# Kernel tuning notes

Hardware: AMD Instinct MI355X
Metric: run time of the kernel (lower is better)

## Reference

```python
import jax, jax.numpy as jnp
import numpy as np

N, T, K, C, O = 2048, 20, 32, 32, 64  # agents, timesteps, neighbors, in_ch, out_ch


def setup_inputs() -> dict:
    key = jax.random.key(0)
    ks = jax.random.split(key, 8)
    s = 0.05
    x = jax.random.normal(ks[0], (N, T, C), dtype=jnp.float32)
    A = jax.random.randint(ks[1], (T, N, K), 0, N)  # neighbor indices into agent dim
    conv_w = jax.random.normal(ks[2], (O, C), jnp.float32) * s  # 1x1 conv == linear [O,C]
    conv_b = jax.random.normal(ks[3], (O,), jnp.float32) * s
    w_ih = jax.random.normal(ks[4], (4 * O, O), jnp.float32) * s  # LSTM gates i,f,g,o
    w_hh = jax.random.normal(ks[5], (4 * O, O), jnp.float32) * s
    b_ih = jax.random.normal(ks[6], (4 * O,), jnp.float32) * s
    b_hh = jax.random.normal(ks[7], (4 * O,), jnp.float32) * s
    return dict(x=x, A=A, conv_w=conv_w, conv_b=conv_b,
                w_ih=w_ih, w_hh=w_hh, b_ih=b_ih, b_hh=b_hh)


def reference(x, A, conv_w, conv_b, w_ih, w_hh, b_ih, b_hh):
    n = x.shape[0]
    xt = jnp.transpose(x, (1, 0, 2))  # [T, N, C]
    # align == 1: per-timestep neighbor gather and relative difference
    gathered = jax.vmap(lambda xs, idx: xs[idx])(xt, A)  # [T, N, K, C]
    diff = gathered - xt[:, :, None, :]  # [T, N, K, C]
    # 1x1 conv (pointwise linear over channels)
    y = jnp.einsum('tnkc,oc->tnko', diff, conv_w) + conv_b  # [T, N, K, O]
    # AdaptiveMaxPool2d((seq_len, 1)): max over the neighbor axis K
    feat = jnp.max(y, axis=2)  # [T, N, O] -- LSTM input (time-major)

    h0 = jnp.zeros((n, O), jnp.float32)
    c0 = jnp.zeros((n, O), jnp.float32)

    def step(carry, x_t):
        h, c = carry
        g = x_t @ w_ih.T + h @ w_hh.T + (b_ih + b_hh)  # [N, 4O]
        i_g, f_g, g_g, o_g = jnp.split(g, 4, axis=-1)
        c = jax.nn.sigmoid(f_g) * c + jax.nn.sigmoid(i_g) * jnp.tanh(g_g)
        h = jax.nn.sigmoid(o_g) * jnp.tanh(c)
        return (h, c), h

    (hN, cN), hs = jax.lax.scan(step, (h0, c0), feat)
    out = jnp.transpose(hs, (1, 0, 2))  # [N, T, O]
    # state_tuple permuted to batch-first as in the torch module
    return out, hN[:, None, :], cN[:, None, :]
```

## Files before the change

kernel.cpp:

```cpp
#include <hip/hip_runtime.h>
#include <hip/hip_bf16.h>
#include <math.h>

#define NA 2048
#define TT 20
#define KK 32
#define CC 32
#define OO 64
#define GG 256

typedef __attribute__((ext_vector_type(8))) short short8;
typedef __attribute__((ext_vector_type(4))) float float4v;

__device__ __forceinline__ float fast_rcp(float x) {
    return __builtin_amdgcn_rcpf(x);
}
__device__ __forceinline__ float sigm(float x) {
    return fast_rcp(1.f + __expf(-x));
}
__device__ __forceinline__ float tanh_fast(float x) {
    return 1.f - 2.f * fast_rcp(1.f + __expf(2.f * x));
}
__device__ __forceinline__ unsigned cvt_rne(float f) {
    unsigned u = __float_as_uint(f);
    return (u + 0x7FFFu + ((u >> 16) & 1u)) >> 16;
}
__device__ __forceinline__ unsigned pack2(float a, float b) {
    return cvt_rne(a) | (cvt_rne(b) << 16);
}
__device__ __forceinline__ float bf_lo(unsigned u) {
    return __uint_as_float(u << 16);
}
__device__ __forceinline__ float bf_hi(unsigned u) {
    return __uint_as_float(u & 0xffff0000u);
}

__global__ __launch_bounds__(256) void proj_kernel(
    const float* __restrict__ x, const float* __restrict__ conv_w,
    const float* __restrict__ conv_b, const float* __restrict__ w_ih,
    const float* __restrict__ w_hh, const float* __restrict__ b_ih,
    const float* __restrict__ b_hh,
    __hip_bfloat16* __restrict__ P, unsigned short* __restrict__ wihb,
    unsigned short* __restrict__ whhb, float* __restrict__ biasT)
{
    const int tid = threadIdx.x;
    if (blockIdx.x == 0) {
        for (int e = tid; e < 4 * OO * OO; e += 256) {
            wihb[e] = (unsigned short)cvt_rne(w_ih[e]);
            whhb[e] = (unsigned short)cvt_rne(w_hh[e]);
        }
        float bj = b_ih[tid] + b_hh[tid];
        #pragma unroll
        for (int o = 0; o < OO; o += 4) {
            float4 cb = *(const float4*)(conv_b + o);
            float4 wr = *(const float4*)(w_ih + (size_t)tid * OO + o);
            bj = fmaf(cb.x, wr.x, bj); bj = fmaf(cb.y, wr.y, bj);
            bj = fmaf(cb.z, wr.z, bj); bj = fmaf(cb.w, wr.w, bj);
        }
        biasT[tid] = bj;
        return;
    }
    const int lane = tid & 63;
    const int wv = tid >> 6;
    float w[CC];
    #pragma unroll
    for (int c = 0; c < CC; c += 4) {
        float4 v = *(const float4*)(conv_w + lane * CC + c);
        w[c] = v.x; w[c + 1] = v.y; w[c + 2] = v.z; w[c + 3] = v.w;
    }
    const int rbase = (blockIdx.x - 1) * 16 + wv * 4;
    #pragma unroll
    for (int i = 0; i < 4; ++i) {
        int r = rbase + i;
        const float* xr = x + (size_t)r * CC;
        float a0 = 0.f, a1 = 0.f;
        #pragma unroll
        for (int c = 0; c < CC; c += 8) {
            float4 v = *(const float4*)(xr + c);
            float4 u = *(const float4*)(xr + c + 4);
            a0 = fmaf(v.x, w[c], a0);     a0 = fmaf(v.y, w[c + 1], a0);
            a0 = fmaf(v.z, w[c + 2], a0); a0 = fmaf(v.w, w[c + 3], a0);
            a1 = fmaf(u.x, w[c + 4], a1); a1 = fmaf(u.y, w[c + 5], a1);
            a1 = fmaf(u.z, w[c + 6], a1); a1 = fmaf(u.w, w[c + 7], a1);
        }
        int n = r / TT;
        int t = r - n * TT;
        ((unsigned short*)P)[(((size_t)t << 11) + n) * OO + lane] =
            (unsigned short)cvt_rne(a0 + a1);
    }
}

__global__ __launch_bounds__(256, 4) void gather_kernel(
    const __hip_bfloat16* __restrict__ P, const int* __restrict__ A,
    unsigned* __restrict__ featw)
{
    __shared__ int A_sh[4][128];
    const int tid = threadIdx.x;
    const int lane = tid & 63;
    const int wv = tid >> 6;
    const int bs = (blockIdx.x & 7) * 320 + (blockIdx.x >> 3);
    const int r0 = bs << 4;
    const int t = r0 >> 11;
    const unsigned short* Pt = (const unsigned short*)P + ((size_t)t << 17);

    const int rw = r0 + wv * 4;
    ((int2*)A_sh[wv])[lane] = ((const int2*)(A + ((size_t)rw << 5)))[lane];

    const int i_row = lane >> 4;
    const int oc8 = lane & 15;
    const char* plane = (const char*)Pt + oc8 * 8;
    const int* myA = &A_sh[wv][i_row * 32];

    const int nself = (rw + i_row) & (NA - 1);
    const uint2 su = *(const uint2*)(plane + ((size_t)nself << 7));

    float m0 = -INFINITY, m1 = -INFINITY, m2 = -INFINITY, m3 = -INFINITY;
    #pragma unroll
    for (int bb = 0; bb < 2; ++bb) {
        int idx[16];
        #pragma unroll
        for (int g = 0; g < 16; ++g)
            idx[g] = myA[bb * 16 + g];
        uint2 uv[16];
        #pragma unroll
        for (int g = 0; g < 16; ++g)
            uv[g] = *(const uint2*)(plane + ((size_t)idx[g] << 7));
        #pragma unroll
        for (int g = 0; g < 16; ++g) {
            m0 = fmaxf(m0, bf_lo(uv[g].x)); m1 = fmaxf(m1, bf_hi(uv[g].x));
            m2 = fmaxf(m2, bf_lo(uv[g].y)); m3 = fmaxf(m3, bf_hi(uv[g].y));
        }
    }
    uint2 pk;
    pk.x = pack2(m0 - bf_lo(su.x), m1 - bf_hi(su.x));
    pk.y = pack2(m2 - bf_lo(su.y), m3 - bf_hi(su.y));
    *(uint2*)&featw[((size_t)(rw + i_row) << 5) + oc8 * 2] = pk;
}

__global__ __launch_bounds__(256) void lstm_kernel(
    const unsigned short* __restrict__ feat,
    const unsigned short* __restrict__ wihb,
    const unsigned short* __restrict__ whhb,
    const float* __restrict__ biasT, float* __restrict__ out)
{
    const int tid = threadIdx.x;
    const int lane = tid & 63;
    const int wv = tid >> 6;
    const int l15 = lane & 15;
    const int q = lane >> 4;
    const int a0 = blockIdx.x * 16;
    const int ch = wv * 16 + l15;

    short8 bfI[4][2], bfH[4][2];
    #pragma unroll
    for (int g = 0; g < 4; ++g) {
        int row = g * 64 + ch;
        #pragma unroll
        for (int ks = 0; ks < 2; ++ks) {
            bfI[g][ks] =
                *(const short8*)(wihb + ((size_t)row << 6) + ks * 32 + q * 8);
            bfH[g][ks] =
                *(const short8*)(whhb + ((size_t)row << 6) + ks * 32 + q * 8);
        }
    }
    float bias_g[4];
    #pragma unroll
    for (int g = 0; g < 4; ++g)
        bias_g[g] = biasT[g * 64 + ch];

    __shared__ __align__(16) unsigned short h_sh[2][16 * 72];

    for (int e = tid; e < 16 * 72 / 2; e += 256)
        ((unsigned*)h_sh[0])[e] = 0u;

    float cst[4] = {0.f, 0.f, 0.f, 0.f};

    short8 ff[2];
    #pragma unroll
    for (int ks = 0; ks < 2; ++ks)
        ff[ks] = *(const short8*)(
            feat + (((size_t)a0 + l15) << 6) + ks * 32 + q * 8);

    __syncthreads();

    for (int t = 0; t < TT; ++t) {
        short8 ah[2];
        #pragma unroll
        for (int ks = 0; ks < 2; ++ks)
            ah[ks] = *(const short8*)(
                &h_sh[t & 1][l15 * 72 + ks * 32 + q * 8]);

        float4v acc[4] = {{0.f, 0.f, 0.f, 0.f}, {0.f, 0.f, 0.f, 0.f},
                          {0.f, 0.f, 0.f, 0.f}, {0.f, 0.f, 0.f, 0.f}};
        #pragma unroll
        for (int ks = 0; ks < 2; ++ks) {
            #pragma unroll
            for (int g = 0; g < 4; ++g) {
                acc[g] = __builtin_amdgcn_mfma_f32_16x16x32_bf16(
                    ff[ks], bfI[g][ks], acc[g], 0, 0, 0);
                acc[g] = __builtin_amdgcn_mfma_f32_16x16x32_bf16(
                    ah[ks], bfH[g][ks], acc[g], 0, 0, 0);
            }
        }

        short8 ffn[2];
        int tn = (t + 1 < TT) ? t + 1 : t;
        #pragma unroll
        for (int ks = 0; ks < 2; ++ks)
            ffn[ks] = *(const short8*)(
                feat + ((((size_t)tn << 11) + a0 + l15) << 6) + ks * 32 + q * 8);

        #pragma unroll
        for (int rg = 0; rg < 4; ++rg) {
            float gi = acc[0][rg] + bias_g[0];
            float gf = acc[1][rg] + bias_g[1];
            float gz = acc[2][rg] + bias_g[2];
            float go = acc[3][rg] + bias_g[3];
            float ig = sigm(gi);
            float fg = sigm(gf);
            float zg = tanh_fast(gz);
            float og = sigm(go);
            cst[rg] = fmaf(fg, cst[rg], ig * zg);
            float hv = og * tanh_fast(cst[rg]);
            int agent = q * 4 + rg;
            h_sh[(t + 1) & 1][agent * 72 + ch] = (unsigned short)cvt_rne(hv);
            out[(((size_t)(a0 + agent) * TT + t) << 6) + ch] = hv;
            if (t == TT - 1) {
                size_t hb = (size_t)NA * TT * OO;
                out[hb + ((size_t)(a0 + agent) << 6) + ch] = hv;
                out[hb + ((size_t)NA << 6) + ((size_t)(a0 + agent) << 6) + ch] =
                    cst[rg];
            }
        }
        __syncthreads();
        ff[0] = ffn[0]; ff[1] = ffn[1];
    }
}

extern "C" void kernel_launch(void* const* d_in, const int* in_sizes, int n_in,
                              void* d_out, int out_size, void* d_ws, size_t ws_size,
                              hipStream_t stream) {
    const float* x      = (const float*)d_in[0];
    const int*   A      = (const int*)  d_in[1];
    const float* conv_w = (const float*)d_in[2];
    const float* conv_b = (const float*)d_in[3];
    const float* w_ih   = (const float*)d_in[4];
    const float* w_hh   = (const float*)d_in[5];
    const float* b_ih   = (const float*)d_in[6];
    const float* b_hh   = (const float*)d_in[7];
    float* out = (float*)d_out;

    char* ws = (char*)d_ws;
    __hip_bfloat16* P  = (__hip_bfloat16*)ws;
    size_t offF = (size_t)TT * NA * OO * 2;
    unsigned* featw = (unsigned*)(ws + offF);
    size_t offW = offF + (size_t)TT * NA * OO * 2;
    unsigned short* wihb = (unsigned short*)(ws + offW);
    unsigned short* whhb = wihb + 4 * OO * OO;
    float* biasT = (float*)(whhb + 4 * OO * OO);

    hipLaunchKernelGGL(proj_kernel, dim3(NA * TT / 16 + 1), dim3(256), 0, stream,
                       x, conv_w, conv_b, w_ih, w_hh, b_ih, b_hh,
                       P, wihb, whhb, biasT);
    hipLaunchKernelGGL(gather_kernel, dim3(NA * TT / 16), dim3(256), 0, stream,
                       P, A, featw);
    hipLaunchKernelGGL(lstm_kernel, dim3(NA / 16), dim3(256), 0, stream,
                       (const unsigned short*)featw, wihb, whhb, biasT, out);
}
```

Measured before the change: 130.2 us.

## Fuse gather and LSTM kernels with per-timestep flags for producer-consumer overlap

Merges the gather and LSTM kernels into one launch. The first NGRP blocks run the recurrent LSTM and spin on per-(timestep, agent-group) flags, and the remaining blocks perform the neighbor gather-max and publish a release flag when each tile is written. The LSTM's early timesteps can then overlap with gathers for later timesteps, and one kernel launch boundary disappears. The cost is spin-wait polling, atomic feature loads, and a reliance on the LSTM blocks and gather blocks being co-resident, which risks deadlock or stalls if the scheduler does not dispatch producers.

```diff
diff --git a/kernel.cpp b/kernel.cpp
--- a/kernel.cpp
+++ b/kernel.cpp
@@ -9,6 +9,10 @@
 #define OO 64
 #define GG 256
 
+#define NGRP (NA / 16)
+#define NGATH (NA * TT / 16)
+#define FLG_STRIDE 32
+
 typedef __attribute__((ext_vector_type(8))) short short8;
 typedef __attribute__((ext_vector_type(4))) float float4v;
 
@@ -33,6 +37,22 @@
 }
 __device__ __forceinline__ float bf_hi(unsigned u) {
     return __uint_as_float(u & 0xffff0000u);
+}
+
+__device__ __forceinline__ void wait_flag(const unsigned* f) {
+    while (__hip_atomic_load(f, __ATOMIC_RELAXED,
+                             __HIP_MEMORY_SCOPE_AGENT) == 0u)
+        __builtin_amdgcn_s_sleep(8);
+}
+__device__ __forceinline__ short8 ld_feat16(const void* p) {
+    const unsigned long long* q = (const unsigned long long*)p;
+    unsigned long long a = __hip_atomic_load(q, __ATOMIC_RELAXED,
+                                             __HIP_MEMORY_SCOPE_AGENT);
+    unsigned long long b = __hip_atomic_load(q + 1, __ATOMIC_RELAXED,
+                                             __HIP_MEMORY_SCOPE_AGENT);
+    union { unsigned long long u[2]; short8 s; } v;
+    v.u[0] = a; v.u[1] = b;
+    return v.s;
 }
 
 __global__ __launch_bounds__(256) void proj_kernel(
@@ -41,7 +61,8 @@
     const float* __restrict__ w_hh, const float* __restrict__ b_ih,
     const float* __restrict__ b_hh,
     __hip_bfloat16* __restrict__ P, unsigned short* __restrict__ wihb,
-    unsigned short* __restrict__ whhb, float* __restrict__ biasT)
+    unsigned short* __restrict__ whhb, float* __restrict__ biasT,
+    unsigned* __restrict__ flags)
 {
     const int tid = threadIdx.x;
     if (blockIdx.x == 0) {
@@ -49,6 +70,8 @@
             wihb[e] = (unsigned short)cvt_rne(w_ih[e]);
             whhb[e] = (unsigned short)cvt_rne(w_hh[e]);
         }
+        for (int g = tid; g < NGATH; g += 256)
+            flags[(size_t)g * FLG_STRIDE] = 0u;
         float bj = b_ih[tid] + b_hh[tid];
         #pragma unroll
         for (int o = 0; o < OO; o += 4) {
@@ -90,65 +113,72 @@
     }
 }
 
-__global__ __launch_bounds__(256, 4) void gather_kernel(
+__global__ __launch_bounds__(256, 4) void gather_lstm_kernel(
     const __hip_bfloat16* __restrict__ P, const int* __restrict__ A,
-    unsigned* __restrict__ featw)
-{
-    __shared__ int A_sh[4][128];
-    const int tid = threadIdx.x;
-    const int lane = tid & 63;
-    const int wv = tid >> 6;
-    const int bs = (blockIdx.x & 7) * 320 + (blockIdx.x >> 3);
-    const int r0 = bs << 4;
-    const int t = r0 >> 11;
-    const unsigned short* Pt = (const unsigned short*)P + ((size_t)t << 17);
-
-    const int rw = r0 + wv * 4;
-    ((int2*)A_sh[wv])[lane] = ((const int2*)(A + ((size_t)rw << 5)))[lane];
-
-    const int i_row = lane >> 4;
-    const int oc8 = lane & 15;
-    const char* plane = (const char*)Pt + oc8 * 8;
-    const int* myA = &A_sh[wv][i_row * 32];
-
-    const int nself = (rw + i_row) & (NA - 1);
-    const uint2 su = *(const uint2*)(plane + ((size_t)nself << 7));
-
-    float m0 = -INFINITY, m1 = -INFINITY, m2 = -INFINITY, m3 = -INFINITY;
-    #pragma unroll
-    for (int bb = 0; bb < 2; ++bb) {
-        int idx[16];
-        #pragma unroll
-        for (int g = 0; g < 16; ++g)
-            idx[g] = myA[bb * 16 + g];
-        uint2 uv[16];
-        #pragma unroll
-        for (int g = 0; g < 16; ++g)
-            uv[g] = *(const uint2*)(plane + ((size_t)idx[g] << 7));
-        #pragma unroll
-        for (int g = 0; g < 16; ++g) {
-            m0 = fmaxf(m0, bf_lo(uv[g].x)); m1 = fmaxf(m1, bf_hi(uv[g].x));
-            m2 = fmaxf(m2, bf_lo(uv[g].y)); m3 = fmaxf(m3, bf_hi(uv[g].y));
-        }
-    }
-    uint2 pk;
-    pk.x = pack2(m0 - bf_lo(su.x), m1 - bf_hi(su.x));
-    pk.y = pack2(m2 - bf_lo(su.y), m3 - bf_hi(su.y));
-    *(uint2*)&featw[((size_t)(rw + i_row) << 5) + oc8 * 2] = pk;
-}
-
-__global__ __launch_bounds__(256) void lstm_kernel(
-    const unsigned short* __restrict__ feat,
+    unsigned* __restrict__ featw,
     const unsigned short* __restrict__ wihb,
     const unsigned short* __restrict__ whhb,
-    const float* __restrict__ biasT, float* __restrict__ out)
+    const float* __restrict__ biasT, unsigned* __restrict__ flags,
+    float* __restrict__ out)
 {
     const int tid = threadIdx.x;
     const int lane = tid & 63;
     const int wv = tid >> 6;
+
+    if (blockIdx.x >= NGRP) {
+        __shared__ int A_sh[4][128];
+        const int gbid = blockIdx.x - NGRP;
+        const int bs = (gbid & 7) * 320 + (gbid >> 3);
+        const int r0 = bs << 4;
+        const int t = r0 >> 11;
+        const unsigned short* Pt =
+            (const unsigned short*)P + ((size_t)t << 17);
+
+        const int rw = r0 + wv * 4;
+        ((int2*)A_sh[wv])[lane] = ((const int2*)(A + ((size_t)rw << 5)))[lane];
+
+        const int i_row = lane >> 4;
+        const int oc8 = lane & 15;
+        const char* plane = (const char*)Pt + oc8 * 8;
+        const int* myA = &A_sh[wv][i_row * 32];
+
+        const int nself = (rw + i_row) & (NA - 1);
+        const uint2 su = *(const uint2*)(plane + ((size_t)nself << 7));
+
+        float m0 = -INFINITY, m1 = -INFINITY;
+        float m2 = -INFINITY, m3 = -INFINITY;
+        #pragma unroll
+        for (int bb = 0; bb < 2; ++bb) {
+            int idx[16];
+            #pragma unroll
+            for (int g = 0; g < 16; ++g)
+                idx[g] = myA[bb * 16 + g];
+            uint2 uv[16];
+            #pragma unroll
+            for (int g = 0; g < 16; ++g)
+                uv[g] = *(const uint2*)(plane + ((size_t)idx[g] << 7));
+            #pragma unroll
+            for (int g = 0; g < 16; ++g) {
+                m0 = fmaxf(m0, bf_lo(uv[g].x)); m1 = fmaxf(m1, bf_hi(uv[g].x));
+                m2 = fmaxf(m2, bf_lo(uv[g].y)); m3 = fmaxf(m3, bf_hi(uv[g].y));
+            }
+        }
+        uint2 pk;
+        pk.x = pack2(m0 - bf_lo(su.x), m1 - bf_hi(su.x));
+        pk.y = pack2(m2 - bf_lo(su.y), m3 - bf_hi(su.y));
+        *(uint2*)&featw[((size_t)(rw + i_row) << 5) + oc8 * 2] = pk;
+
+        __syncthreads();
+        if (tid == 0)
+            __hip_atomic_store(flags + (size_t)bs * FLG_STRIDE, 1u,
+                               __ATOMIC_RELEASE, __HIP_MEMORY_SCOPE_AGENT);
+        return;
+    }
+
     const int l15 = lane & 15;
     const int q = lane >> 4;
-    const int a0 = blockIdx.x * 16;
+    const int bid = blockIdx.x;
+    const int a0 = bid * 16;
     const int ch = wv * 16 + l15;
 
     short8 bfI[4][2], bfH[4][2];
@@ -175,11 +205,15 @@
 
     float cst[4] = {0.f, 0.f, 0.f, 0.f};
 
+    const unsigned short* feat = (const unsigned short*)featw;
+
+    wait_flag(flags + (size_t)(0 * NGRP + bid) * FLG_STRIDE);
     short8 ff[2];
     #pragma unroll
     for (int ks = 0; ks < 2; ++ks)
-        ff[ks] = *(const short8*)(
-            feat + (((size_t)a0 + l15) << 6) + ks * 32 + q * 8);
+        ff[ks] = ld_feat16(feat + (((size_t)a0 + l15) << 6) + ks * 32 + q * 8);
+    if (TT > 1)
+        wait_flag(flags + (size_t)(1 * NGRP + bid) * FLG_STRIDE);
 
     __syncthreads();
 
@@ -207,8 +241,10 @@
         int tn = (t + 1 < TT) ? t + 1 : t;
         #pragma unroll
         for (int ks = 0; ks < 2; ++ks)
-            ffn[ks] = *(const short8*)(
+            ffn[ks] = ld_feat16(
                 feat + ((((size_t)tn << 11) + a0 + l15) << 6) + ks * 32 + q * 8);
+        if (t + 2 < TT)
+            wait_flag(flags + (size_t)((t + 2) * NGRP + bid) * FLG_STRIDE);
 
         #pragma unroll
         for (int rg = 0; rg < 4; ++rg) {
@@ -258,12 +294,11 @@
     unsigned short* wihb = (unsigned short*)(ws + offW);
     unsigned short* whhb = wihb + 4 * OO * OO;
     float* biasT = (float*)(whhb + 4 * OO * OO);
+    unsigned* flags = (unsigned*)(ws + offW + 65536 + 1024);
 
     hipLaunchKernelGGL(proj_kernel, dim3(NA * TT / 16 + 1), dim3(256), 0, stream,
                        x, conv_w, conv_b, w_ih, w_hh, b_ih, b_hh,
-                       P, wihb, whhb, biasT);
-    hipLaunchKernelGGL(gather_kernel, dim3(NA * TT / 16), dim3(256), 0, stream,
-                       P, A, featw);
-    hipLaunchKernelGGL(lstm_kernel, dim3(NA / 16), dim3(256), 0, stream,
-                       (const unsigned short*)featw, wihb, whhb, biasT, out);
-}
+                       P, wihb, whhb, biasT, flags);
+    hipLaunchKernelGGL(gather_lstm_kernel, dim3(NGRP + NGATH), dim3(256), 0,
+                       stream, P, A, featw, wihb, whhb, biasT, flags, out);
+}
```

After: 195.2 us. 1.5x slower.

## Fuse projection, gather and LSTM into one cooperative kernel with grid syncs

Applied to the files above, without the earlier changes.

Merges the three kernels into a single persistent cooperative kernel of 512 blocks. Projection and gather loop over work items in grid-stride fashion, with grid.sync between stages, and only the first 128 blocks run the LSTM recurrence. This removes two kernel launch boundaries and their tail gaps. In exchange it adds grid-wide barrier cost, caps occupancy at 512 resident blocks, and runs the LSTM on a small subset of blocks. It falls back to the old three-kernel path if a cooperative launch is not possible.

```diff
diff --git a/kernel.cpp b/kernel.cpp
--- a/kernel.cpp
+++ b/kernel.cpp
@@ -1,6 +1,9 @@
 #include <hip/hip_runtime.h>
 #include <hip/hip_bf16.h>
+#include <hip/hip_cooperative_groups.h>
 #include <math.h>
+
+namespace cg = cooperative_groups;
 
 #define NA 2048
 #define TT 20
@@ -9,6 +12,11 @@
 #define OO 64
 #define GG 256
 
+#define NGRP (NA / 16)
+#define NGATH (NA * TT / 16)
+#define NB 512
+#define NCU 256
+
 typedef __attribute__((ext_vector_type(8))) short short8;
 typedef __attribute__((ext_vector_type(4))) float float4v;
 
@@ -35,16 +43,24 @@
     return __uint_as_float(u & 0xffff0000u);
 }
 
-__global__ __launch_bounds__(256) void proj_kernel(
-    const float* __restrict__ x, const float* __restrict__ conv_w,
-    const float* __restrict__ conv_b, const float* __restrict__ w_ih,
-    const float* __restrict__ w_hh, const float* __restrict__ b_ih,
-    const float* __restrict__ b_hh,
-    __hip_bfloat16* __restrict__ P, unsigned short* __restrict__ wihb,
-    unsigned short* __restrict__ whhb, float* __restrict__ biasT)
+__global__ __launch_bounds__(256, 2) void mega_kernel(
+    const float* __restrict__ x, const int* __restrict__ A,
+    const float* __restrict__ conv_w, const float* __restrict__ conv_b,
+    const float* __restrict__ w_ih, const float* __restrict__ w_hh,
+    const float* __restrict__ b_ih, const float* __restrict__ b_hh,
+    __hip_bfloat16* __restrict__ P, unsigned* __restrict__ featw,
+    unsigned short* __restrict__ wihb, unsigned short* __restrict__ whhb,
+    float* __restrict__ biasT, float* __restrict__ out)
 {
+    cg::grid_group grid = cg::this_grid();
     const int tid = threadIdx.x;
-    if (blockIdx.x == 0) {
+    const int lane = tid & 63;
+    const int wv = tid >> 6;
+
+    __shared__ int A_sh[4][128];
+    __shared__ __align__(16) unsigned short h_sh[2][16 * 72];
+
+    if (blockIdx.x == NB - 1) {
         for (int e = tid; e < 4 * OO * OO; e += 256) {
             wihb[e] = (unsigned short)cvt_rne(w_ih[e]);
             whhb[e] = (unsigned short)cvt_rne(w_hh[e]);
@@ -58,94 +74,84 @@
             bj = fmaf(cb.z, wr.z, bj); bj = fmaf(cb.w, wr.w, bj);
         }
         biasT[tid] = bj;
-        return;
-    }
-    const int lane = tid & 63;
-    const int wv = tid >> 6;
-    float w[CC];
-    #pragma unroll
-    for (int c = 0; c < CC; c += 4) {
-        float4 v = *(const float4*)(conv_w + lane * CC + c);
-        w[c] = v.x; w[c + 1] = v.y; w[c + 2] = v.z; w[c + 3] = v.w;
-    }
-    const int rbase = (blockIdx.x - 1) * 16 + wv * 4;
-    #pragma unroll
-    for (int i = 0; i < 4; ++i) {
-        int r = rbase + i;
-        const float* xr = x + (size_t)r * CC;
-        float a0 = 0.f, a1 = 0.f;
-        #pragma unroll
-        for (int c = 0; c < CC; c += 8) {
-            float4 v = *(const float4*)(xr + c);
-            float4 u = *(const float4*)(xr + c + 4);
-            a0 = fmaf(v.x, w[c], a0);     a0 = fmaf(v.y, w[c + 1], a0);
-            a0 = fmaf(v.z, w[c + 2], a0); a0 = fmaf(v.w, w[c + 3], a0);
-            a1 = fmaf(u.x, w[c + 4], a1); a1 = fmaf(u.y, w[c + 5], a1);
-            a1 = fmaf(u.z, w[c + 6], a1); a1 = fmaf(u.w, w[c + 7], a1);
-        }
-        int n = r / TT;
-        int t = r - n * TT;
-        ((unsigned short*)P)[(((size_t)t << 11) + n) * OO + lane] =
-            (unsigned short)cvt_rne(a0 + a1);
-    }
-}
-
-__global__ __launch_bounds__(256, 4) void gather_kernel(
-    const __hip_bfloat16* __restrict__ P, const int* __restrict__ A,
-    unsigned* __restrict__ featw)
-{
-    __shared__ int A_sh[4][128];
-    const int tid = threadIdx.x;
-    const int lane = tid & 63;
-    const int wv = tid >> 6;
-    const int bs = (blockIdx.x & 7) * 320 + (blockIdx.x >> 3);
-    const int r0 = bs << 4;
-    const int t = r0 >> 11;
-    const unsigned short* Pt = (const unsigned short*)P + ((size_t)t << 17);
-
-    const int rw = r0 + wv * 4;
-    ((int2*)A_sh[wv])[lane] = ((const int2*)(A + ((size_t)rw << 5)))[lane];
-
-    const int i_row = lane >> 4;
-    const int oc8 = lane & 15;
-    const char* plane = (const char*)Pt + oc8 * 8;
-    const int* myA = &A_sh[wv][i_row * 32];
-
-    const int nself = (rw + i_row) & (NA - 1);
-    const uint2 su = *(const uint2*)(plane + ((size_t)nself << 7));
-
-    float m0 = -INFINITY, m1 = -INFINITY, m2 = -INFINITY, m3 = -INFINITY;
-    #pragma unroll
-    for (int bb = 0; bb < 2; ++bb) {
-        int idx[16];
-        #pragma unroll
-        for (int g = 0; g < 16; ++g)
-            idx[g] = myA[bb * 16 + g];
-        uint2 uv[16];
-        #pragma unroll
-        for (int g = 0; g < 16; ++g)
-            uv[g] = *(const uint2*)(plane + ((size_t)idx[g] << 7));
-        #pragma unroll
-        for (int g = 0; g < 16; ++g) {
-            m0 = fmaxf(m0, bf_lo(uv[g].x)); m1 = fmaxf(m1, bf_hi(uv[g].x));
-            m2 = fmaxf(m2, bf_lo(uv[g].y)); m3 = fmaxf(m3, bf_hi(uv[g].y));
-        }
-    }
-    uint2 pk;
-    pk.x = pack2(m0 - bf_lo(su.x), m1 - bf_hi(su.x));
-    pk.y = pack2(m2 - bf_lo(su.y), m3 - bf_hi(su.y));
-    *(uint2*)&featw[((size_t)(rw + i_row) << 5) + oc8 * 2] = pk;
-}
-
-__global__ __launch_bounds__(256) void lstm_kernel(
-    const unsigned short* __restrict__ feat,
-    const unsigned short* __restrict__ wihb,
-    const unsigned short* __restrict__ whhb,
-    const float* __restrict__ biasT, float* __restrict__ out)
-{
-    const int tid = threadIdx.x;
-    const int lane = tid & 63;
-    const int wv = tid >> 6;
+    }
+    {
+        float w[CC];
+        #pragma unroll
+        for (int c = 0; c < CC; c += 4) {
+            float4 v = *(const float4*)(conv_w + lane * CC + c);
+            w[c] = v.x; w[c + 1] = v.y; w[c + 2] = v.z; w[c + 3] = v.w;
+        }
+        for (int item = blockIdx.x; item < NGATH; item += NB) {
+            const int rbase = item * 16 + wv * 4;
+            #pragma unroll
+            for (int i = 0; i < 4; ++i) {
+                int r = rbase + i;
+                const float* xr = x + (size_t)r * CC;
+                float a0 = 0.f, a1 = 0.f;
+                #pragma unroll
+                for (int c = 0; c < CC; c += 8) {
+                    float4 v = *(const float4*)(xr + c);
+                    float4 u = *(const float4*)(xr + c + 4);
+                    a0 = fmaf(v.x, w[c], a0);     a0 = fmaf(v.y, w[c + 1], a0);
+                    a0 = fmaf(v.z, w[c + 2], a0); a0 = fmaf(v.w, w[c + 3], a0);
+                    a1 = fmaf(u.x, w[c + 4], a1); a1 = fmaf(u.y, w[c + 5], a1);
+                    a1 = fmaf(u.z, w[c + 6], a1); a1 = fmaf(u.w, w[c + 7], a1);
+                }
+                int n = r / TT;
+                int t = r - n * TT;
+                ((unsigned short*)P)[(((size_t)t << 11) + n) * OO + lane] =
+                    (unsigned short)cvt_rne(a0 + a1);
+            }
+        }
+    }
+    grid.sync();
+
+    for (int item = blockIdx.x; item < NGATH; item += NB) {
+        const int bs = (item & 7) * 320 + (item >> 3);
+        const int r0 = bs << 4;
+        const int t = r0 >> 11;
+        const unsigned short* Pt =
+            (const unsigned short*)P + ((size_t)t << 17);
+
+        const int rw = r0 + wv * 4;
+        ((int2*)A_sh[wv])[lane] = ((const int2*)(A + ((size_t)rw << 5)))[lane];
+
+        const int i_row = lane >> 4;
+        const int oc8 = lane & 15;
+        const char* plane = (const char*)Pt + oc8 * 8;
+        const int* myA = &A_sh[wv][i_row * 32];
+
+        const int nself = (rw + i_row) & (NA - 1);
+        const uint2 su = *(const uint2*)(plane + ((size_t)nself << 7));
+
+        float m0 = -INFINITY, m1 = -INFINITY;
+        float m2 = -INFINITY, m3 = -INFINITY;
+        #pragma unroll
+        for (int bb = 0; bb < 2; ++bb) {
+            int idx[16];
+            #pragma unroll
+            for (int g = 0; g < 16; ++g)
+                idx[g] = myA[bb * 16 + g];
+            uint2 uv[16];
+            #pragma unroll
+            for (int g = 0; g < 16; ++g)
+                uv[g] = *(const uint2*)(plane + ((size_t)idx[g] << 7));
+            #pragma unroll
+            for (int g = 0; g < 16; ++g) {
+                m0 = fmaxf(m0, bf_lo(uv[g].x)); m1 = fmaxf(m1, bf_hi(uv[g].x));
+                m2 = fmaxf(m2, bf_lo(uv[g].y)); m3 = fmaxf(m3, bf_hi(uv[g].y));
+            }
+        }
+        uint2 pk;
+        pk.x = pack2(m0 - bf_lo(su.x), m1 - bf_hi(su.x));
+        pk.y = pack2(m2 - bf_lo(su.y), m3 - bf_hi(su.y));
+        *(uint2*)&featw[((size_t)(rw + i_row) << 5) + oc8 * 2] = pk;
+    }
+    grid.sync();
+
+    if (blockIdx.x >= NGRP) return;
+
     const int l15 = lane & 15;
     const int q = lane >> 4;
     const int a0 = blockIdx.x * 16;
@@ -168,12 +174,11 @@
     for (int g = 0; g < 4; ++g)
         bias_g[g] = biasT[g * 64 + ch];
 
-    __shared__ __align__(16) unsigned short h_sh[2][16 * 72];
-
     for (int e = tid; e < 16 * 72 / 2; e += 256)
         ((unsigned*)h_sh[0])[e] = 0u;
 
     float cst[4] = {0.f, 0.f, 0.f, 0.f};
+    const unsigned short* feat = (const unsigned short*)featw;
 
     short8 ff[2];
     #pragma unroll
@@ -237,6 +242,208 @@
     }
 }
 
+__global__ __launch_bounds__(256) void proj_kernel(
+    const float* __restrict__ x, const float* __restrict__ conv_w,
+    const float* __restrict__ conv_b, const float* __restrict__ w_ih,
+    const float* __restrict__ w_hh, const float* __restrict__ b_ih,
+    const float* __restrict__ b_hh,
+    __hip_bfloat16* __restrict__ P, unsigned short* __restrict__ wihb,
+    unsigned short* __restrict__ whhb, float* __restrict__ biasT)
+{
+    const int tid = threadIdx.x;
+    if (blockIdx.x == 0) {
+        for (int e = tid; e < 4 * OO * OO; e += 256) {
+            wihb[e] = (unsigned short)cvt_rne(w_ih[e]);
+            whhb[e] = (unsigned short)cvt_rne(w_hh[e]);
+        }
+        float bj = b_ih[tid] + b_hh[tid];
+        #pragma unroll
+        for (int o = 0; o < OO; o += 4) {
+            float4 cb = *(const float4*)(conv_b + o);
+            float4 wr = *(const float4*)(w_ih + (size_t)tid * OO + o);
+            bj = fmaf(cb.x, wr.x, bj); bj = fmaf(cb.y, wr.y, bj);
+            bj = fmaf(cb.z, wr.z, bj); bj = fmaf(cb.w, wr.w, bj);
+        }
+        biasT[tid] = bj;
+        return;
+    }
+    const int lane = tid & 63;
+    const int wv = tid >> 6;
+    float w[CC];
+    #pragma unroll
+    for (int c = 0; c < CC; c += 4) {
+        float4 v = *(const float4*)(conv_w + lane * CC + c);
+        w[c] = v.x; w[c + 1] = v.y; w[c + 2] = v.z; w[c + 3] = v.w;
+    }
+    const int rbase = (blockIdx.x - 1) * 16 + wv * 4;
+    #pragma unroll
+    for (int i = 0; i < 4; ++i) {
+        int r = rbase + i;
+        const float* xr = x + (size_t)r * CC;
+        float a0 = 0.f, a1 = 0.f;
+        #pragma unroll
+        for (int c = 0; c < CC; c += 8) {
+            float4 v = *(const float4*)(xr + c);
+            float4 u = *(const float4*)(xr + c + 4);
+            a0 = fmaf(v.x, w[c], a0);     a0 = fmaf(v.y, w[c + 1], a0);
+            a0 = fmaf(v.z, w[c + 2], a0); a0 = fmaf(v.w, w[c + 3], a0);
+            a1 = fmaf(u.x, w[c + 4], a1); a1 = fmaf(u.y, w[c + 5], a1);
+            a1 = fmaf(u.z, w[c + 6], a1); a1 = fmaf(u.w, w[c + 7], a1);
+        }
+        int n = r / TT;
+        int t = r - n * TT;
+        ((unsigned short*)P)[(((size_t)t << 11) + n) * OO + lane] =
+            (unsigned short)cvt_rne(a0 + a1);
+    }
+}
+
+__global__ __launch_bounds__(256, 4) void gather_kernel(
+    const __hip_bfloat16* __restrict__ P, const int* __restrict__ A,
+    unsigned* __restrict__ featw)
+{
+    __shared__ int A_sh[4][128];
+    const int tid = threadIdx.x;
+    const int lane = tid & 63;
+    const int wv = tid >> 6;
+    const int bs = (blockIdx.x & 7) * 320 + (blockIdx.x >> 3);
+    const int r0 = bs << 4;
+    const int t = r0 >> 11;
+    const unsigned short* Pt = (const unsigned short*)P + ((size_t)t << 17);
+
+    const int rw = r0 + wv * 4;
+    ((int2*)A_sh[wv])[lane] = ((const int2*)(A + ((size_t)rw << 5)))[lane];
+
+    const int i_row = lane >> 4;
+    const int oc8 = lane & 15;
+    const char* plane = (const char*)Pt + oc8 * 8;
+    const int* myA = &A_sh[wv][i_row * 32];
+
+    const int nself = (rw + i_row) & (NA - 1);
+    const uint2 su = *(const uint2*)(plane + ((size_t)nself << 7));
+
+    float m0 = -INFINITY, m1 = -INFINITY, m2 = -INFINITY, m3 = -INFINITY;
+    #pragma unroll
+    for (int bb = 0; bb < 2; ++bb) {
+        int idx[16];
+        #pragma unroll
+        for (int g = 0; g < 16; ++g)
+            idx[g] = myA[bb * 16 + g];
+        uint2 uv[16];
+        #pragma unroll
+        for (int g = 0; g < 16; ++g)
+            uv[g] = *(const uint2*)(plane + ((size_t)idx[g] << 7));
+        #pragma unroll
+        for (int g = 0; g < 16; ++g) {
+            m0 = fmaxf(m0, bf_lo(uv[g].x)); m1 = fmaxf(m1, bf_hi(uv[g].x));
+            m2 = fmaxf(m2, bf_lo(uv[g].y)); m3 = fmaxf(m3, bf_hi(uv[g].y));
+        }
+    }
+    uint2 pk;
+    pk.x = pack2(m0 - bf_lo(su.x), m1 - bf_hi(su.x));
+    pk.y = pack2(m2 - bf_lo(su.y), m3 - bf_hi(su.y));
+    *(uint2*)&featw[((size_t)(rw + i_row) << 5) + oc8 * 2] = pk;
+}
+
+__global__ __launch_bounds__(256) void lstm_kernel(
+    const unsigned short* __restrict__ feat,
+    const unsigned short* __restrict__ wihb,
+    const unsigned short* __restrict__ whhb,
+    const float* __restrict__ biasT, float* __restrict__ out)
+{
+    const int tid = threadIdx.x;
+    const int lane = tid & 63;
+    const int wv = tid >> 6;
+    const int l15 = lane & 15;
+    const int q = lane >> 4;
+    const int a0 = blockIdx.x * 16;
+    const int ch = wv * 16 + l15;
+
+    short8 bfI[4][2], bfH[4][2];
+    #pragma unroll
+    for (int g = 0; g < 4; ++g) {
+        int row = g * 64 + ch;
+        #pragma unroll
+        for (int ks = 0; ks < 2; ++ks) {
+            bfI[g][ks] =
+                *(const short8*)(wihb + ((size_t)row << 6) + ks * 32 + q * 8);
+            bfH[g][ks] =
+                *(const short8*)(whhb + ((size_t)row << 6) + ks * 32 + q * 8);
+        }
+    }
+    float bias_g[4];
+    #pragma unroll
+    for (int g = 0; g < 4; ++g)
+        bias_g[g] = biasT[g * 64 + ch];
+
+    __shared__ __align__(16) unsigned short h_sh[2][16 * 72];
+
+    for (int e = tid; e < 16 * 72 / 2; e += 256)
+        ((unsigned*)h_sh[0])[e] = 0u;
+
+    float cst[4] = {0.f, 0.f, 0.f, 0.f};
+
+    short8 ff[2];
+    #pragma unroll
+    for (int ks = 0; ks < 2; ++ks)
+        ff[ks] = *(const short8*)(
+            feat + (((size_t)a0 + l15) << 6) + ks * 32 + q * 8);
+
+    __syncthreads();
+
+    for (int t = 0; t < TT; ++t) {
+        short8 ah[2];
+        #pragma unroll
+        for (int ks = 0; ks < 2; ++ks)
+            ah[ks] = *(const short8*)(
+                &h_sh[t & 1][l15 * 72 + ks * 32 + q * 8]);
+
+        float4v acc[4] = {{0.f, 0.f, 0.f, 0.f}, {0.f, 0.f, 0.f, 0.f},
+                          {0.f, 0.f, 0.f, 0.f}, {0.f, 0.f, 0.f, 0.f}};
+        #pragma unroll
+        for (int ks = 0; ks < 2; ++ks) {
+            #pragma unroll
+            for (int g = 0; g < 4; ++g) {
+                acc[g] = __builtin_amdgcn_mfma_f32_16x16x32_bf16(
+                    ff[ks], bfI[g][ks], acc[g], 0, 0, 0);
+                acc[g] = __builtin_amdgcn_mfma_f32_16x16x32_bf16(
+                    ah[ks], bfH[g][ks], acc[g], 0, 0, 0);
+            }
+        }
+
+        short8 ffn[2];
+        int tn = (t + 1 < TT) ? t + 1 : t;
+        #pragma unroll
+        for (int ks = 0; ks < 2; ++ks)
+            ffn[ks] = *(const short8*)(
+                feat + ((((size_t)tn << 11) + a0 + l15) << 6) + ks * 32 + q * 8);
+
+        #pragma unroll
+        for (int rg = 0; rg < 4; ++rg) {
+            float gi = acc[0][rg] + bias_g[0];
+            float gf = acc[1][rg] + bias_g[1];
+            float gz = acc[2][rg] + bias_g[2];
+            float go = acc[3][rg] + bias_g[3];
+            float ig = sigm(gi);
+            float fg = sigm(gf);
+            float zg = tanh_fast(gz);
+            float og = sigm(go);
+            cst[rg] = fmaf(fg, cst[rg], ig * zg);
+            float hv = og * tanh_fast(cst[rg]);
+            int agent = q * 4 + rg;
+            h_sh[(t + 1) & 1][agent * 72 + ch] = (unsigned short)cvt_rne(hv);
+            out[(((size_t)(a0 + agent) * TT + t) << 6) + ch] = hv;
+            if (t == TT - 1) {
+                size_t hb = (size_t)NA * TT * OO;
+                out[hb + ((size_t)(a0 + agent) << 6) + ch] = hv;
+                out[hb + ((size_t)NA << 6) + ((size_t)(a0 + agent) << 6) + ch] =
+                    cst[rg];
+            }
+        }
+        __syncthreads();
+        ff[0] = ffn[0]; ff[1] = ffn[1];
+    }
+}
+
 extern "C" void kernel_launch(void* const* d_in, const int* in_sizes, int n_in,
                               void* d_out, int out_size, void* d_ws, size_t ws_size,
                               hipStream_t stream) {
@@ -259,11 +466,34 @@
     unsigned short* whhb = wihb + 4 * OO * OO;
     float* biasT = (float*)(whhb + 4 * OO * OO);
 
-    hipLaunchKernelGGL(proj_kernel, dim3(NA * TT / 16 + 1), dim3(256), 0, stream,
-                       x, conv_w, conv_b, w_ih, w_hh, b_ih, b_hh,
-                       P, wihb, whhb, biasT);
-    hipLaunchKernelGGL(gather_kernel, dim3(NA * TT / 16), dim3(256), 0, stream,
-                       P, A, featw);
-    hipLaunchKernelGGL(lstm_kernel, dim3(NA / 16), dim3(256), 0, stream,
-                       (const unsigned short*)featw, wihb, whhb, biasT, out);
-}
+    static int coop_state = 0;
+    if (coop_state == 0) {
+        int maxb = 0;
+        hipError_t e = hipOccupancyMaxActiveBlocksPerMultiprocessor(
+            &maxb, (const void*)mega_kernel, 256, 0);
+        coop_state = (e == hipSuccess && maxb * NCU >= NB) ? 1 : -1;
+    }
+
+    bool done = false;
+    if (coop_state == 1) {
+        void* args[] = {&x, &A, &conv_w, &conv_b, &w_ih, &w_hh, &b_ih, &b_hh,
+                        &P, &featw, &wihb, &whhb, &biasT, &out};
+        hipError_t e = hipLaunchCooperativeKernel(
+            (const void*)mega_kernel, dim3(NB), dim3(256), args, 0, stream);
+        if (e == hipSuccess) {
+            done = true;
+        } else {
+            coop_state = -1;
+        }
+    }
+
+    if (!done) {
+        hipLaunchKernelGGL(proj_kernel, dim3(NGATH + 1), dim3(256), 0, stream,
+                           x, conv_w, conv_b, w_ih, w_hh, b_ih, b_hh,
+                           P, wihb, whhb, biasT);
+        hipLaunchKernelGGL(gather_kernel, dim3(NGATH), dim3(256), 0, stream,
+                           P, A, featw);
+        hipLaunchKernelGGL(lstm_kernel, dim3(NA / 16), dim3(256), 0, stream,
+                           (const unsigned short*)featw, wihb, whhb, biasT, out);
+    }
+}
```

Result: slower. 251.9 us (+93.4%).
